# Optimization experiments

Measured on AMD Instinct MI355X. Metric: run time of the kernel, lower is better.

## Reference

```python
import jax, jax.numpy as jnp
import numpy as np

SINKHORN_ALPHA = 0.05
OT_MAX_ITER = 100
STOP_THR = 0.005
EPS = 1e-16
N_TOPICS, VOCAB, DIM = 1024, 50000, 256


def setup_inputs() -> dict:
    key = jax.random.key(0)
    k1, k2 = jax.random.split(key)
    x = jax.random.uniform(k1, (N_TOPICS, DIM), dtype=jnp.float32)
    y = jax.random.uniform(k2, (VOCAB, DIM), dtype=jnp.float32)
    return {"x": x, "y": y}


def _pairwise_sq_euclidean(x, y):
    return (jnp.sum(x * x, axis=1, keepdims=True)
            + jnp.sum(y * y, axis=1)
            - 2.0 * (x @ y.T))


def reference(x, y):
    M = _pairwise_sq_euclidean(x, y)          # [n, m]
    n, m = M.shape
    dt = M.dtype
    a = jnp.full((n, 1), 1.0 / n, dtype=dt)    # uniform source marginal
    b = jnp.full((m, 1), 1.0 / m, dtype=dt)    # uniform target marginal
    K = jnp.exp(-M * SINKHORN_ALPHA)           # Gibbs kernel [n, m]
    u0 = jnp.full((n, 1), 1.0 / n, dtype=dt)
    v0 = jnp.zeros((m, 1), dtype=dt)

    def cond_fn(carry):
        u, v, err, cpt = carry
        return (err > STOP_THR) & (cpt < OT_MAX_ITER)

    def body_fn(carry):
        u, v, err, cpt = carry
        v = b / (K.T @ u + EPS)                # [m, 1]
        u = a / (K @ v + EPS)                  # [n, 1]
        cpt = cpt + 1

        def compute_err(_):
            bb = v * (K.T @ u)                 # current column marginal
            return jnp.max(jnp.sum(jnp.abs(bb - b), axis=0))

        # original: convergence check only when cpt % 50 == 1
        err = jax.lax.cond((cpt % 50) == 1, compute_err, lambda _: err, operand=None)
        return (u, v, err, cpt)

    init = (u0, v0, jnp.asarray(1.0, dt), jnp.asarray(0, jnp.int32))
    u, v, err, cpt = jax.lax.while_loop(cond_fn, body_fn, init)

    transp = u * (K * v.T)                     # transport plan [n, m]
    loss_etp = jnp.sum(transp * M)
    return (loss_etp, transp)
```

## Files before the change

kernel.cpp:

```cpp
#include <hip/hip_runtime.h>
#include <hip/hip_cooperative_groups.h>
#include <cstdint>

namespace cg = cooperative_groups;

#define N_T 1024
#define M_V 50000
#define DIMS 256
#define NPAD 50048
#define GPANELS 391
#define CBLK 196
#define NPART (CBLK * 64)
#define NCHUNK 782
#define COOP_BLOCKS 1024
#define J4TOT 12500
#define FBLK 49
#define LPART (FBLK * 64)

constexpr float ALPHA     = 0.05f;
constexpr float INV_ALPHA = 20.0f;
constexpr float A_VAL     = 1.0f / 1024.0f;
constexpr float B_VAL     = 1.0f / 50000.0f;
constexpr float THR       = 0.005f;
constexpr float EPSV      = 1e-16f;

typedef short    bf16x8 __attribute__((ext_vector_type(8)));
typedef float    f32x4  __attribute__((ext_vector_type(4)));
typedef _Float16 half8v __attribute__((ext_vector_type(8)));
typedef _Float16 half4v __attribute__((ext_vector_type(4)));

__device__ __forceinline__ float blockReduce256(float val) {
  #pragma unroll
  for (int off = 32; off; off >>= 1) val += __shfl_down(val, off, 64);
  __shared__ float redw[4];
  int lane = threadIdx.x & 63;
  int wid  = threadIdx.x >> 6;
  if (lane == 0) redw[wid] = val;
  __syncthreads();
  float r = 0.0f;
  if (threadIdx.x == 0) r = redw[0] + redw[1] + redw[2] + redw[3];
  __syncthreads();
  return r;
}

__device__ __forceinline__ unsigned short f2bf(float f) {
  union { float f; unsigned u; } c{f};
  unsigned r = c.u + 0x7FFF + ((c.u >> 16) & 1);
  return (unsigned short)(r >> 16);
}
__device__ __forceinline__ float bf2f(unsigned short b) {
  union { unsigned u; float f; } c{(unsigned)b << 16};
  return c.f;
}

__device__ __forceinline__ void gload16(const void* g, void* l) {
  __builtin_amdgcn_global_load_lds((const __attribute__((address_space(1))) unsigned int*)g,
                                   (__attribute__((address_space(3))) unsigned int*)l, 16, 0, 0);
}

__global__ __launch_bounds__(256) void sumsq_kernel(const float* __restrict__ in,
                                                    float* __restrict__ o, int rows) {
  int r = blockIdx.x;
  if (r >= rows) return;
  float v = in[(size_t)r * DIMS + threadIdx.x];
  float s = blockReduce256(v * v);
  if (threadIdx.x == 0) o[r] = s;
}

__global__ __launch_bounds__(256) void pack_x_kernel(const float* __restrict__ x,
                                                     unsigned short* __restrict__ Ap) {
  int r = blockIdx.x * 2 + (threadIdx.x >> 7);
  int k = (threadIdx.x & 127) * 2;
  float2 vx = *(const float2*)&x[(size_t)r * DIMS + k];
  ushort2 h2, l2;
  h2.x = f2bf(vx.x); h2.y = f2bf(vx.y);
  l2.x = f2bf(vx.x - bf2f(h2.x)); l2.y = f2bf(vx.y - bf2f(h2.y));
  *(ushort2*)&Ap[(size_t)r * 512 + k]       = h2;
  *(ushort2*)&Ap[(size_t)r * 512 + 256 + k] = l2;
}

__global__ __launch_bounds__(256) void pack_y_kernel(const float* __restrict__ y,
                                                     unsigned short* __restrict__ Bp) {
  int r = blockIdx.x * 2 + (threadIdx.x >> 7);
  int k = (threadIdx.x & 127) * 2;
  ushort2 h2 = {0, 0};
  if (r < M_V) {
    float2 vy = *(const float2*)&y[(size_t)r * DIMS + k];
    h2.x = f2bf(vy.x); h2.y = f2bf(vy.y);
  }
  *(ushort2*)&Bp[(size_t)r * 256 + k] = h2;
}

__global__ __launch_bounds__(256) void mfma_gemm_kernel(const unsigned short* __restrict__ Ap,
                                                        const unsigned short* __restrict__ Bp,
                                                        const float* __restrict__ xx,
                                                        const float* __restrict__ yy,
                                                        _Float16* __restrict__ Kh,
                                                        float* __restrict__ colsumPart) {
  const int t  = blockIdx.x & 63;
  const int gb = blockIdx.x >> 6;
  const int panel = gb * 8 + (t & 7);
  const int rt    = t >> 3;
  if (panel >= GPANELS) return;
  const int i0 = rt * 128;
  const int j0 = panel * 128;

  __shared__ unsigned short Ah[128][32];
  __shared__ unsigned short Al[128][32];
  __shared__ unsigned short Bs[128][32];
  const int tid  = threadIdx.x;
  const int lane = tid & 63;
  const int wid  = tid >> 6;
  const int wr = wid >> 1, wc = wid & 1;

  f32x4 acc[4][4];
  #pragma unroll
  for (int m = 0; m < 4; ++m)
    #pragma unroll
    for (int n = 0; n < 4; ++n) acc[m][n] = (f32x4){0.f, 0.f, 0.f, 0.f};

  const int srow  = lane >> 2;
  const int sslot = lane & 3;

  for (int k0 = 0; k0 < 256; k0 += 32) {
    #pragma unroll
    for (int q = 0; q < 2; ++q) {
      int rbase = (wid * 2 + q) * 16;
      int row = rbase + srow;
      int cg_ = sslot ^ ((row >> 1) & 3);
      gload16(Ap + (size_t)(i0 + row) * 512 + k0 + cg_ * 8,       &Ah[rbase][0]);
      gload16(Ap + (size_t)(i0 + row) * 512 + 256 + k0 + cg_ * 8, &Al[rbase][0]);
      gload16(Bp + (size_t)(j0 + row) * 256 + k0 + cg_ * 8,       &Bs[rbase][0]);
    }
    __syncthreads();
    bf16x8 ah[4], al[4], bb[4];
    #pragma unroll
    for (int m = 0; m < 4; ++m) {
      int row = wr * 64 + m * 16 + (lane & 15);
      int sl  = (lane >> 4) ^ ((row >> 1) & 3);
      ah[m] = *(const bf16x8*)&Ah[row][sl * 8];
      al[m] = *(const bf16x8*)&Al[row][sl * 8];
    }
    #pragma unroll
    for (int n = 0; n < 4; ++n) {
      int col = wc * 64 + n * 16 + (lane & 15);
      int sl  = (lane >> 4) ^ ((col >> 1) & 3);
      bb[n] = *(const bf16x8*)&Bs[col][sl * 8];
    }
    #pragma unroll
    for (int m = 0; m < 4; ++m)
      #pragma unroll
      for (int n = 0; n < 4; ++n) {
        acc[m][n] = __builtin_amdgcn_mfma_f32_16x16x32_bf16(ah[m], bb[n], acc[m][n], 0, 0, 0);
        acc[m][n] = __builtin_amdgcn_mfma_f32_16x16x32_bf16(al[m], bb[n], acc[m][n], 0, 0, 0);
      }
    __syncthreads();
  }

  float csum[4] = {0.f, 0.f, 0.f, 0.f};
  #pragma unroll
  for (int m = 0; m < 4; ++m) {
    int rowb = i0 + wr * 64 + m * 16 + (lane >> 4) * 4;
    #pragma unroll
    for (int n = 0; n < 4; ++n) {
      int col = j0 + wc * 64 + n * 16 + (lane & 15);
      float yyc = (col < M_V) ? yy[col] : 0.0f;
      #pragma unroll
      for (int r = 0; r < 4; ++r) {
        float mval = xx[rowb + r] + yyc - 2.0f * acc[m][n][r];
        _Float16 kh = (_Float16)__expf(-ALPHA * mval);
        if (col < M_V) Kh[(size_t)(rowb + r) * M_V + col] = kh;
        csum[n] += (float)kh;
      }
    }
  }
  #pragma unroll
  for (int n = 0; n < 4; ++n) {
    float c = csum[n];
    c += __shfl_xor(c, 16, 64);
    c += __shfl_xor(c, 32, 64);
    if (lane < 16) {
      int col = j0 + wc * 64 + n * 16 + lane;
      colsumPart[(size_t)(rt * 2 + wr) * NPAD + col] = c;
    }
  }
}

#define BM 64
#define BN 64
#define BK 32
__global__ __launch_bounds__(256) void gemm_k_kernel(const float* __restrict__ x,
                                                     const float* __restrict__ y,
                                                     const float* __restrict__ xx,
                                                     const float* __restrict__ yy,
                                                     float* Kmat) {
  __shared__ float As[BK][BM];
  __shared__ float Bs[BK][BN + 1];
  int tid = threadIdx.x;
  int i0 = blockIdx.y * BM;
  int j0 = blockIdx.x * BN;
  int tx = tid & 15, ty = tid >> 4;
  float acc[4][4] = {};
  for (int k0 = 0; k0 < DIMS; k0 += BK) {
    #pragma unroll
    for (int l = tid; l < 512; l += 256) {
      int r = l >> 3, kq = l & 7;
      float4 a4 = *(const float4*)&x[(size_t)(i0 + r) * DIMS + k0 + kq * 4];
      As[kq * 4 + 0][r] = a4.x; As[kq * 4 + 1][r] = a4.y;
      As[kq * 4 + 2][r] = a4.z; As[kq * 4 + 3][r] = a4.w;
    }
    #pragma unroll
    for (int l = tid; l < 512; l += 256) {
      int r = l >> 3, kq = l & 7;
      int j = j0 + r;
      float4 b4 = make_float4(0.f, 0.f, 0.f, 0.f);
      if (j < M_V) b4 = *(const float4*)&y[(size_t)j * DIMS + k0 + kq * 4];
      Bs[kq * 4 + 0][r] = b4.x; Bs[kq * 4 + 1][r] = b4.y;
      Bs[kq * 4 + 2][r] = b4.z; Bs[kq * 4 + 3][r] = b4.w;
    }
    __syncthreads();
    #pragma unroll
    for (int k = 0; k < BK; ++k) {
      float a[4], b[4];
      #pragma unroll
      for (int r = 0; r < 4; ++r) a[r] = As[k][ty * 4 + r];
      #pragma unroll
      for (int c = 0; c < 4; ++c) b[c] = Bs[k][tx * 4 + c];
      #pragma unroll
      for (int r = 0; r < 4; ++r)
        #pragma unroll
        for (int c = 0; c < 4; ++c) acc[r][c] += a[r] * b[c];
    }
    __syncthreads();
  }
  #pragma unroll
  for (int r = 0; r < 4; ++r) {
    int i = i0 + ty * 4 + r;
    float xxi = xx[i];
    #pragma unroll
    for (int c = 0; c < 4; ++c) {
      int j = j0 + tx * 4 + c;
      if (j < M_V) {
        float m = xxi + yy[j] - 2.0f * acc[r][c];
        Kmat[(size_t)i * M_V + j] = __expf(-ALPHA * m);
      }
    }
  }
}

__global__ __launch_bounds__(256) void v1_kernel(const float* __restrict__ cp,
                                                 float* __restrict__ v,
                                                 float* __restrict__ errAcc) {
  int j = blockIdx.x * 256 + threadIdx.x;
  if (j == 0) errAcc[0] = 0.0f;
  if (j < M_V) {
    float s = 0.0f;
    #pragma unroll
    for (int q = 0; q < 16; ++q) s += cp[(size_t)q * NPAD + j];
    v[j] = B_VAL / (s * A_VAL + EPSV);
  }
}

__global__ __launch_bounds__(256) void rowpass_kernel(const _Float16* __restrict__ Kh,
                                                      const float* __restrict__ v,
                                                      float* __restrict__ rowPart) {
  const int i = blockIdx.y;
  const int c = blockIdx.x;
  const half8v* K8 = (const half8v*)(Kh + (size_t)i * M_V);
  const float4* v4 = (const float4*)v;
  float p = 0.0f;
  int q = c * 3125 + threadIdx.x;
  #pragma unroll
  for (int it = 0; it < 12; ++it, q += 256) {
    half8v k8 = K8[q];
    float4 va = v4[q * 2], vb = v4[q * 2 + 1];
    p += (float)k8[0] * va.x + (float)k8[1] * va.y + (float)k8[2] * va.z + (float)k8[3] * va.w
       + (float)k8[4] * vb.x + (float)k8[5] * vb.y + (float)k8[6] * vb.z + (float)k8[7] * vb.w;
  }
  if (threadIdx.x < 53) {
    int q2 = c * 3125 + 3072 + threadIdx.x;
    half8v k8 = K8[q2];
    float4 va = v4[q2 * 2], vb = v4[q2 * 2 + 1];
    p += (float)k8[0] * va.x + (float)k8[1] * va.y + (float)k8[2] * va.z + (float)k8[3] * va.w
       + (float)k8[4] * vb.x + (float)k8[5] * vb.y + (float)k8[6] * vb.z + (float)k8[7] * vb.w;
  }
  p = blockReduce256(p);
  if (threadIdx.x == 0) rowPart[c * N_T + i] = p;
}

__global__ void u_kernel(const float* __restrict__ rowPart, float* __restrict__ u) {
  int i = blockIdx.x * 256 + threadIdx.x;
  u[i] = A_VAL / (rowPart[i] + rowPart[N_T + i] + EPSV);
}

__global__ __launch_bounds__(256) void specfinal_kernel(const _Float16* __restrict__ Kh,
                                                        const float* __restrict__ u_,
                                                        const float* __restrict__ v_,
                                                        float* __restrict__ out,
                                                        float* __restrict__ sPart,
                                                        float* __restrict__ lossPart) {
  const int j4 = blockIdx.x * 256 + threadIdx.x;
  const int by = blockIdx.y;
  float contrib = 0.0f;
  if (j4 < J4TOT) {
    float4 vv = ((const float4*)v_)[j4];
    float4 sp = {0.f, 0.f, 0.f, 0.f};
    const size_t jb = (size_t)j4 * 4;
    #pragma unroll
    for (int r = 0; r < 16; ++r) {
      int i = by * 16 + r;
      half4v k4 = *(const half4v*)(Kh + (size_t)i * M_V + jb);
      float kx = (float)k4[0], ky = (float)k4[1], kz = (float)k4[2], kw = (float)k4[3];
      float ui = u_[i];
      float tx_ = ui * kx * vv.x, ty_ = ui * ky * vv.y;
      float tz_ = ui * kz * vv.z, tw_ = ui * kw * vv.w;
      size_t o = 1 + (size_t)i * M_V + jb;
      out[o] = tx_; out[o + 1] = ty_; out[o + 2] = tz_; out[o + 3] = tw_;
      contrib += tx_ * (-__logf(kx)) + ty_ * (-__logf(ky))
               + tz_ * (-__logf(kz)) + tw_ * (-__logf(kw));
      sp.x += kx * ui; sp.y += ky * ui; sp.z += kz * ui; sp.w += kw * ui;
    }
    ((float4*)(sPart + (size_t)by * M_V))[j4] = sp;
  }
  contrib = blockReduce256(contrib) * INV_ALPHA;
  if (threadIdx.x == 0) lossPart[by * FBLK + blockIdx.x] = contrib;
}

__global__ __launch_bounds__(256) void errfinish_kernel(const float* __restrict__ sPart,
                                                        const float* __restrict__ v_,
                                                        float* errAcc) {
  int j = blockIdx.x * 256 + threadIdx.x;
  float e = 0.0f;
  if (j < M_V) {
    float s = 0.0f;
    #pragma unroll
    for (int q = 0; q < 64; ++q) s += sPart[(size_t)q * M_V + j];
    e = fabsf(v_[j] * s - B_VAL);
  }
  e = blockReduce256(e);
  if (threadIdx.x == 0) atomicAdd(errAcc, e);
}

__global__ void setflag_kernel(const float* errAcc, int* notconv) {
  *notconv = (errAcc[0] > THR) ? 1 : 0;
}
__global__ void set1_kernel(int* p) { *p = 1; }

__global__ __launch_bounds__(256) void finishloss_kernel(const float* __restrict__ lossPart,
                                                         float* out, int np_) {
  float s = 0.0f;
  for (int i = threadIdx.x; i < np_; i += 256) s += lossPart[i];
  s = blockReduce256(s);
  if (threadIdx.x == 0) out[0] = s;
}

template <typename KT>
__global__ __launch_bounds__(256, 4) void sinkhorn_coop(const KT* Km,
                                                        float* __restrict__ u,
                                                        float* __restrict__ v,
                                                        float* __restrict__ s,
                                                        float* __restrict__ errAcc,
                                                        const int* __restrict__ notconv) {
  if (*notconv == 0) return;
  cg::grid_group grid = cg::this_grid();
  __shared__ float su[N_T];
  __shared__ float red[8][64];
  const int tid = threadIdx.x;
  const int bid = blockIdx.x;
  {
    int g0 = bid * 256 + tid;
    if (g0 < N_T) u[g0] = A_VAL;
    if (g0 < 2) errAcc[g0] = 0.0f;
  }
  grid.sync();
  for (int t = 1; t <= 100; ++t) {
    const bool check = (t == 2) || (t == 52);
    for (int i = tid; i < N_T; i += 256) su[i] = u[i];
    __syncthreads();
    const int g = tid >> 5, jl = tid & 31;
    float eacc = 0.0f;
    for (int c = bid; c < NCHUNK; c += COOP_BLOCKS) {
      const int j0 = c * 64;
      const int jj = j0 + jl * 2;
      float p0 = 0.f, p1 = 0.f;
      if (jj < M_V) {
        const KT* base = Km + (size_t)(g * 128) * M_V + jj;
        #pragma unroll 4
        for (int i = 0; i < 128; ++i) {
          float k0 = (float)base[(size_t)i * M_V];
          float k1 = (float)base[(size_t)i * M_V + 1];
          float uu = su[g * 128 + i];
          p0 += k0 * uu; p1 += k1 * uu;
        }
      }
      red[g][jl * 2]     = p0;
      red[g][jl * 2 + 1] = p1;
      __syncthreads();
      if (tid < 64) {
        int j = j0 + tid;
        if (j < M_V) {
          float st = 0.f;
          #pragma unroll
          for (int q = 0; q < 8; ++q) st += red[q][tid];
          if (check) {
            s[j] = st;
            eacc += fabsf(v[j] * st - B_VAL);
          } else {
            v[j] = B_VAL / (st + EPSV);
          }
        }
      }
      __syncthreads();
    }
    if (check) {
      float e = blockReduce256(eacc);
      if (tid == 0) atomicAdd(&errAcc[t == 2 ? 0 : 1], e);
    }
    grid.sync();
    if (check) {
      float e = errAcc[t == 2 ? 0 : 1];
      if (e <= THR) break;
      if (tid < 64) {
        for (int c = bid; c < NCHUNK; c += COOP_BLOCKS) {
          int j = c * 64 + tid;
          if (j < M_V) v[j] = B_VAL / (s[j] + EPSV);
        }
      }
      grid.sync();
    }
    {
      int i = bid;
      float p = 0.f;
      if (i < N_T) {
        const KT* row = Km + (size_t)i * M_V;
        for (int j = tid; j < M_V; j += 256) p += (float)row[j] * v[j];
      }
      p = blockReduce256(p);
      if (tid == 0 && i < N_T) u[i] = A_VAL / (p + EPSV);
    }
    grid.sync();
  }
}

template <typename KT>
__global__ __launch_bounds__(256) void final_kernel(const KT* Kmat,
                                                    const float* __restrict__ u,
                                                    const float* __restrict__ v,
                                                    float* out,
                                                    float* __restrict__ partials,
                                                    const int* __restrict__ gate) {
  if (*gate == 0) return;
  int j = blockIdx.x * 256 + threadIdx.x;
  float contrib = 0.0f;
  if (j < M_V) {
    float vj = v[j];
    #pragma unroll 4
    for (int r = 0; r < 16; ++r) {
      int i = blockIdx.y * 16 + r;
      size_t idx = (size_t)i * M_V + j;
      float k = (float)Kmat[idx];
      float tr = u[i] * k * vj;
      float m = -__logf(k) * INV_ALPHA;
      out[1 + idx] = tr;
      contrib += tr * m;
    }
  }
  contrib = blockReduce256(contrib);
  if (threadIdx.x == 0) partials[blockIdx.y * gridDim.x + blockIdx.x] = contrib;
}

__global__ __launch_bounds__(256) void finish_kernel(const float* __restrict__ partials,
                                                     float* out, int np_,
                                                     const int* __restrict__ gate) {
  if (*gate == 0) return;
  float s = 0.0f;
  for (int i = threadIdx.x; i < np_; i += 256) s += partials[i];
  s = blockReduce256(s);
  if (threadIdx.x == 0) out[0] = s;
}

extern "C" void kernel_launch(void* const* d_in, const int* in_sizes, int n_in,
                              void* d_out, int out_size, void* d_ws, size_t ws_size,
                              hipStream_t stream) {
  const float* x = (const float*)d_in[0];
  const float* y = (const float*)d_in[1];
  float* out = (float*)d_out;

  uintptr_t wp = (uintptr_t)d_ws;
  uintptr_t wend = (uintptr_t)d_ws + ws_size;
  auto alloc = [&](size_t bytes) -> void* {
    wp = (wp + 255) & ~(uintptr_t)255;
    void* p = (void*)wp;
    wp += bytes;
    return p;
  };
  float* u        = (float*)alloc((size_t)N_T * 4);
  float* v        = (float*)alloc((size_t)M_V * 4);
  float* s        = (float*)alloc((size_t)M_V * 4);
  float* xx       = (float*)alloc((size_t)N_T * 4);
  float* yy       = (float*)alloc((size_t)M_V * 4);
  float* partials = (float*)alloc((size_t)NPART * 4);
  float* lossPart = (float*)alloc((size_t)LPART * 4);
  float* rowPart  = (float*)alloc((size_t)2 * N_T * 4);
  float* errAcc   = (float*)alloc(64);
  int*   notconv  = (int*)alloc(64);
  float* colsumPart = (float*)alloc((size_t)16 * NPAD * 4);
  float* sPart    = (float*)alloc((size_t)64 * M_V * 4);

  const size_t apbytes = (size_t)N_T * 512 * 2;
  const size_t bpbytes = (size_t)NPAD * 256 * 2;
  const size_t khbytes = (size_t)N_T * M_V * 2;
  const size_t kfbytes = (size_t)N_T * M_V * 4;

  bool fast = ((wp + 1024) + apbytes + bpbytes + khbytes) <= wend;

  sumsq_kernel<<<N_T, 256, 0, stream>>>(x, xx, N_T);
  sumsq_kernel<<<M_V, 256, 0, stream>>>(y, yy, M_V);

  if (fast) {
    unsigned short* Ap = (unsigned short*)alloc(apbytes);
    unsigned short* Bp = (unsigned short*)alloc(bpbytes);
    _Float16*       Kh = (_Float16*)alloc(khbytes);

    pack_x_kernel<<<N_T / 2, 256, 0, stream>>>(x, Ap);
    pack_y_kernel<<<NPAD / 2, 256, 0, stream>>>(y, Bp);
    mfma_gemm_kernel<<<49 * 64, 256, 0, stream>>>(Ap, Bp, xx, yy, Kh, colsumPart);

    v1_kernel<<<CBLK, 256, 0, stream>>>(colsumPart, v, errAcc);
    rowpass_kernel<<<dim3(2, N_T), 256, 0, stream>>>(Kh, v, rowPart);
    u_kernel<<<N_T / 256, 256, 0, stream>>>(rowPart, u);

    specfinal_kernel<<<dim3(FBLK, 64), 256, 0, stream>>>(Kh, u, v, out, sPart, lossPart);
    errfinish_kernel<<<CBLK, 256, 0, stream>>>(sPart, v, errAcc);
    setflag_kernel<<<1, 1, 0, stream>>>(errAcc, notconv);
    finishloss_kernel<<<1, 256, 0, stream>>>(lossPart, out, LPART);

    void* coopArgs[] = {(void*)&Kh, (void*)&u, (void*)&v, (void*)&s,
                        (void*)&errAcc, (void*)&notconv};
    hipLaunchCooperativeKernel(reinterpret_cast<void*>(sinkhorn_coop<_Float16>),
                               dim3(COOP_BLOCKS), dim3(256), coopArgs, 0, stream);
    final_kernel<_Float16><<<dim3(CBLK, 64), 256, 0, stream>>>(Kh, u, v, out, partials, notconv);
    finish_kernel<<<1, 256, 0, stream>>>(partials, out, NPART, notconv);
  } else {
    bool k_in_ws = ((wp + 512) + kfbytes) <= wend;
    float* Kmat = k_in_ws ? (float*)alloc(kfbytes) : out + 1;
    gemm_k_kernel<<<dim3((M_V + BN - 1) / BN, N_T / BM), 256, 0, stream>>>(x, y, xx, yy, Kmat);
    set1_kernel<<<1, 1, 0, stream>>>(notconv);
    void* coopArgs[] = {(void*)&Kmat, (void*)&u, (void*)&v, (void*)&s,
                        (void*)&errAcc, (void*)&notconv};
    hipLaunchCooperativeKernel(reinterpret_cast<void*>(sinkhorn_coop<float>),
                               dim3(COOP_BLOCKS), dim3(256), coopArgs, 0, stream);
    final_kernel<float><<<dim3(CBLK, 64), 256, 0, stream>>>(Kmat, u, v, out, partials, notconv);
    finish_kernel<<<1, 256, 0, stream>>>(partials, out, NPART, notconv);
  }
}
```

Before: 305.2 us.

## Double-buffer GEMM LDS loads, fuse sum-of-squares into pack kernels, widen specfinal

The MFMA GEMM now double-buffers its LDS tiles, issuing the next k-slice's global-to-LDS loads before computing the current one, with explicit waitcnt and barrier control. This is meant to hide load latency behind compute. The row sum-of-squares for x and y is folded into the pack kernels, which removes two separate passes over the inputs. specfinal now handles 8 columns per thread instead of 4, for wider half loads and fewer blocks. In exchange, the GEMM uses twice the LDS and relies on hand-written waitcnt counts for correctness.

```diff
diff --git a/kernel.cpp b/kernel.cpp
--- a/kernel.cpp
+++ b/kernel.cpp
@@ -13,9 +13,9 @@
 #define NPART (CBLK * 64)
 #define NCHUNK 782
 #define COOP_BLOCKS 1024
-#define J4TOT 12500
-#define FBLK 49
-#define LPART (FBLK * 64)
+#define J8TOT 6250
+#define F8BLK 25
+#define LPART (F8BLK * 64)
 
 constexpr float ALPHA     = 0.05f;
 constexpr float INV_ALPHA = 20.0f;
@@ -27,7 +27,6 @@
 typedef short    bf16x8 __attribute__((ext_vector_type(8)));
 typedef float    f32x4  __attribute__((ext_vector_type(4)));
 typedef _Float16 half8v __attribute__((ext_vector_type(8)));
-typedef _Float16 half4v __attribute__((ext_vector_type(4)));
 
 __device__ __forceinline__ float blockReduce256(float val) {
   #pragma unroll
@@ -68,7 +67,8 @@
 }
 
 __global__ __launch_bounds__(256) void pack_x_kernel(const float* __restrict__ x,
-                                                     unsigned short* __restrict__ Ap) {
+                                                     unsigned short* __restrict__ Ap,
+                                                     float* __restrict__ xx) {
   int r = blockIdx.x * 2 + (threadIdx.x >> 7);
   int k = (threadIdx.x & 127) * 2;
   float2 vx = *(const float2*)&x[(size_t)r * DIMS + k];
@@ -77,18 +77,36 @@
   l2.x = f2bf(vx.x - bf2f(h2.x)); l2.y = f2bf(vx.y - bf2f(h2.y));
   *(ushort2*)&Ap[(size_t)r * 512 + k]       = h2;
   *(ushort2*)&Ap[(size_t)r * 512 + 256 + k] = l2;
+  float ssq = vx.x * vx.x + vx.y * vx.y;
+  #pragma unroll
+  for (int off = 32; off; off >>= 1) ssq += __shfl_down(ssq, off, 64);
+  __shared__ float rr[4];
+  int lane = threadIdx.x & 63, wid = threadIdx.x >> 6;
+  if (lane == 0) rr[wid] = ssq;
+  __syncthreads();
+  if ((threadIdx.x & 127) == 0) xx[r] = rr[wid] + rr[wid + 1];
 }
 
 __global__ __launch_bounds__(256) void pack_y_kernel(const float* __restrict__ y,
-                                                     unsigned short* __restrict__ Bp) {
+                                                     unsigned short* __restrict__ Bp,
+                                                     float* __restrict__ yy) {
   int r = blockIdx.x * 2 + (threadIdx.x >> 7);
   int k = (threadIdx.x & 127) * 2;
   ushort2 h2 = {0, 0};
+  float ssq = 0.0f;
   if (r < M_V) {
     float2 vy = *(const float2*)&y[(size_t)r * DIMS + k];
     h2.x = f2bf(vy.x); h2.y = f2bf(vy.y);
+    ssq = vy.x * vy.x + vy.y * vy.y;
   }
   *(ushort2*)&Bp[(size_t)r * 256 + k] = h2;
+  #pragma unroll
+  for (int off = 32; off; off >>= 1) ssq += __shfl_down(ssq, off, 64);
+  __shared__ float rr[4];
+  int lane = threadIdx.x & 63, wid = threadIdx.x >> 6;
+  if (lane == 0) rr[wid] = ssq;
+  __syncthreads();
+  if ((threadIdx.x & 127) == 0 && r < M_V) yy[r] = rr[wid] + rr[wid + 1];
 }
 
 __global__ __launch_bounds__(256) void mfma_gemm_kernel(const unsigned short* __restrict__ Ap,
@@ -105,9 +123,9 @@
   const int i0 = rt * 128;
   const int j0 = panel * 128;
 
-  __shared__ unsigned short Ah[128][32];
-  __shared__ unsigned short Al[128][32];
-  __shared__ unsigned short Bs[128][32];
+  __shared__ unsigned short Ah[2][128][32];
+  __shared__ unsigned short Al[2][128][32];
+  __shared__ unsigned short Bs[2][128][32];
   const int tid  = threadIdx.x;
   const int lane = tid & 63;
   const int wid  = tid >> 6;
@@ -122,30 +140,43 @@
   const int srow  = lane >> 2;
   const int sslot = lane & 3;
 
-  for (int k0 = 0; k0 < 256; k0 += 32) {
+  auto STAGE = [&](int b, int k0) {
     #pragma unroll
     for (int q = 0; q < 2; ++q) {
       int rbase = (wid * 2 + q) * 16;
       int row = rbase + srow;
       int cg_ = sslot ^ ((row >> 1) & 3);
-      gload16(Ap + (size_t)(i0 + row) * 512 + k0 + cg_ * 8,       &Ah[rbase][0]);
-      gload16(Ap + (size_t)(i0 + row) * 512 + 256 + k0 + cg_ * 8, &Al[rbase][0]);
-      gload16(Bp + (size_t)(j0 + row) * 256 + k0 + cg_ * 8,       &Bs[rbase][0]);
-    }
-    __syncthreads();
+      gload16(Ap + (size_t)(i0 + row) * 512 + k0 + cg_ * 8,       &Ah[b][rbase][0]);
+      gload16(Ap + (size_t)(i0 + row) * 512 + 256 + k0 + cg_ * 8, &Al[b][rbase][0]);
+      gload16(Bp + (size_t)(j0 + row) * 256 + k0 + cg_ * 8,       &Bs[b][rbase][0]);
+    }
+  };
+
+  STAGE(0, 0);
+  int cur = 0;
+  #pragma unroll
+  for (int step = 0; step < 8; ++step) {
+    if (step < 7) {
+      STAGE(cur ^ 1, (step + 1) * 32);
+      asm volatile("s_waitcnt vmcnt(6)" ::: "memory");
+    } else {
+      asm volatile("s_waitcnt vmcnt(0)" ::: "memory");
+    }
+    __builtin_amdgcn_s_barrier();
+    __builtin_amdgcn_sched_barrier(0);
     bf16x8 ah[4], al[4], bb[4];
     #pragma unroll
     for (int m = 0; m < 4; ++m) {
       int row = wr * 64 + m * 16 + (lane & 15);
       int sl  = (lane >> 4) ^ ((row >> 1) & 3);
-      ah[m] = *(const bf16x8*)&Ah[row][sl * 8];
-      al[m] = *(const bf16x8*)&Al[row][sl * 8];
+      ah[m] = *(const bf16x8*)&Ah[cur][row][sl * 8];
+      al[m] = *(const bf16x8*)&Al[cur][row][sl * 8];
     }
     #pragma unroll
     for (int n = 0; n < 4; ++n) {
       int col = wc * 64 + n * 16 + (lane & 15);
       int sl  = (lane >> 4) ^ ((col >> 1) & 3);
-      bb[n] = *(const bf16x8*)&Bs[col][sl * 8];
+      bb[n] = *(const bf16x8*)&Bs[cur][col][sl * 8];
     }
     #pragma unroll
     for (int m = 0; m < 4; ++m)
@@ -154,7 +185,10 @@
         acc[m][n] = __builtin_amdgcn_mfma_f32_16x16x32_bf16(ah[m], bb[n], acc[m][n], 0, 0, 0);
         acc[m][n] = __builtin_amdgcn_mfma_f32_16x16x32_bf16(al[m], bb[n], acc[m][n], 0, 0, 0);
       }
-    __syncthreads();
+    asm volatile("s_waitcnt lgkmcnt(0)" ::: "memory");
+    __builtin_amdgcn_sched_barrier(0);
+    __builtin_amdgcn_s_barrier();
+    cur ^= 1;
   }
 
   float csum[4] = {0.f, 0.f, 0.f, 0.f};
@@ -299,31 +333,38 @@
                                                         float* __restrict__ out,
                                                         float* __restrict__ sPart,
                                                         float* __restrict__ lossPart) {
-  const int j4 = blockIdx.x * 256 + threadIdx.x;
+  const int j8 = blockIdx.x * 256 + threadIdx.x;
   const int by = blockIdx.y;
   float contrib = 0.0f;
-  if (j4 < J4TOT) {
-    float4 vv = ((const float4*)v_)[j4];
-    float4 sp = {0.f, 0.f, 0.f, 0.f};
-    const size_t jb = (size_t)j4 * 4;
+  if (j8 < J8TOT) {
+    const size_t jb = (size_t)j8 * 8;
+    float4 va = ((const float4*)v_)[j8 * 2];
+    float4 vb = ((const float4*)v_)[j8 * 2 + 1];
+    float sp0 = 0.f, sp1 = 0.f, sp2 = 0.f, sp3 = 0.f;
+    float sp4 = 0.f, sp5 = 0.f, sp6 = 0.f, sp7 = 0.f;
     #pragma unroll
     for (int r = 0; r < 16; ++r) {
       int i = by * 16 + r;
-      half4v k4 = *(const half4v*)(Kh + (size_t)i * M_V + jb);
-      float kx = (float)k4[0], ky = (float)k4[1], kz = (float)k4[2], kw = (float)k4[3];
+      half8v k8 = *(const half8v*)(Kh + (size_t)i * M_V + jb);
       float ui = u_[i];
-      float tx_ = ui * kx * vv.x, ty_ = ui * ky * vv.y;
-      float tz_ = ui * kz * vv.z, tw_ = ui * kw * vv.w;
+      float k0 = (float)k8[0], k1 = (float)k8[1], k2 = (float)k8[2], k3 = (float)k8[3];
+      float k4 = (float)k8[4], k5 = (float)k8[5], k6 = (float)k8[6], k7 = (float)k8[7];
+      float t0 = ui * k0 * va.x, t1 = ui * k1 * va.y, t2 = ui * k2 * va.z, t3 = ui * k3 * va.w;
+      float t4 = ui * k4 * vb.x, t5 = ui * k5 * vb.y, t6 = ui * k6 * vb.z, t7 = ui * k7 * vb.w;
       size_t o = 1 + (size_t)i * M_V + jb;
-      out[o] = tx_; out[o + 1] = ty_; out[o + 2] = tz_; out[o + 3] = tw_;
-      contrib += tx_ * (-__logf(kx)) + ty_ * (-__logf(ky))
-               + tz_ * (-__logf(kz)) + tw_ * (-__logf(kw));
-      sp.x += kx * ui; sp.y += ky * ui; sp.z += kz * ui; sp.w += kw * ui;
-    }
-    ((float4*)(sPart + (size_t)by * M_V))[j4] = sp;
+      out[o]     = t0; out[o + 1] = t1; out[o + 2] = t2; out[o + 3] = t3;
+      out[o + 4] = t4; out[o + 5] = t5; out[o + 6] = t6; out[o + 7] = t7;
+      contrib += t0 * (-__logf(k0)) + t1 * (-__logf(k1)) + t2 * (-__logf(k2)) + t3 * (-__logf(k3))
+               + t4 * (-__logf(k4)) + t5 * (-__logf(k5)) + t6 * (-__logf(k6)) + t7 * (-__logf(k7));
+      sp0 += k0 * ui; sp1 += k1 * ui; sp2 += k2 * ui; sp3 += k3 * ui;
+      sp4 += k4 * ui; sp5 += k5 * ui; sp6 += k6 * ui; sp7 += k7 * ui;
+    }
+    float* sb = sPart + (size_t)by * M_V + jb;
+    *(float4*)sb       = make_float4(sp0, sp1, sp2, sp3);
+    *(float4*)(sb + 4) = make_float4(sp4, sp5, sp6, sp7);
   }
   contrib = blockReduce256(contrib) * INV_ALPHA;
-  if (threadIdx.x == 0) lossPart[by * FBLK + blockIdx.x] = contrib;
+  if (threadIdx.x == 0) lossPart[by * F8BLK + blockIdx.x] = contrib;
 }
 
 __global__ __launch_bounds__(256) void errfinish_kernel(const float* __restrict__ sPart,
@@ -514,23 +555,20 @@
 
   bool fast = ((wp + 1024) + apbytes + bpbytes + khbytes) <= wend;
 
-  sumsq_kernel<<<N_T, 256, 0, stream>>>(x, xx, N_T);
-  sumsq_kernel<<<M_V, 256, 0, stream>>>(y, yy, M_V);
-
   if (fast) {
     unsigned short* Ap = (unsigned short*)alloc(apbytes);
     unsigned short* Bp = (unsigned short*)alloc(bpbytes);
     _Float16*       Kh = (_Float16*)alloc(khbytes);
 
-    pack_x_kernel<<<N_T / 2, 256, 0, stream>>>(x, Ap);
-    pack_y_kernel<<<NPAD / 2, 256, 0, stream>>>(y, Bp);
+    pack_x_kernel<<<N_T / 2, 256, 0, stream>>>(x, Ap, xx);
+    pack_y_kernel<<<NPAD / 2, 256, 0, stream>>>(y, Bp, yy);
     mfma_gemm_kernel<<<49 * 64, 256, 0, stream>>>(Ap, Bp, xx, yy, Kh, colsumPart);
 
     v1_kernel<<<CBLK, 256, 0, stream>>>(colsumPart, v, errAcc);
     rowpass_kernel<<<dim3(2, N_T), 256, 0, stream>>>(Kh, v, rowPart);
     u_kernel<<<N_T / 256, 256, 0, stream>>>(rowPart, u);
 
-    specfinal_kernel<<<dim3(FBLK, 64), 256, 0, stream>>>(Kh, u, v, out, sPart, lossPart);
+    specfinal_kernel<<<dim3(F8BLK, 64), 256, 0, stream>>>(Kh, u, v, out, sPart, lossPart);
     errfinish_kernel<<<CBLK, 256, 0, stream>>>(sPart, v, errAcc);
     setflag_kernel<<<1, 1, 0, stream>>>(errAcc, notconv);
     finishloss_kernel<<<1, 256, 0, stream>>>(lossPart, out, LPART);
@@ -542,6 +580,8 @@
     final_kernel<_Float16><<<dim3(CBLK, 64), 256, 0, stream>>>(Kh, u, v, out, partials, notconv);
     finish_kernel<<<1, 256, 0, stream>>>(partials, out, NPART, notconv);
   } else {
+    sumsq_kernel<<<N_T, 256, 0, stream>>>(x, xx, N_T);
+    sumsq_kernel<<<M_V, 256, 0, stream>>>(y, yy, M_V);
     bool k_in_ws = ((wp + 512) + kfbytes) <= wend;
     float* Kmat = k_in_ws ? (float*)alloc(kfbytes) : out + 1;
     gemm_k_kernel<<<dim3((M_V + BN - 1) / BN, N_T / BM), 256, 0, stream>>>(x, y, xx, yy, Kmat);
```

New measurement: 273.3 us. 10.4% less time.
